# Performance work log

Hardware: AMD Instinct MI355X
Metric: run time of the kernel (lower is better)

Reference implementation:

```python
import jax, jax.numpy as jnp
import numpy as np

B, C_IN, C_OUT, L = 16, 128, 128, 1024
DK, DV, H = 32, 32, 8
SCALE = DK ** (-0.5)


def setup_inputs() -> dict:
    key = jax.random.key(0)
    ks = jax.random.split(key, 7)
    qkv_dim = H * (2 * DK + DV)
    # Conv1d with kernel_size=1 == per-position linear; store weights as (out, in)
    return {
        "x": jax.random.normal(ks[0], (B, C_IN, L), dtype=jnp.float32),
        "w_qkv": jax.random.normal(ks[1], (qkv_dim, C_IN), dtype=jnp.float32) * (C_IN ** -0.5),
        "b_qkv": jax.random.normal(ks[2], (qkv_dim,), dtype=jnp.float32) * 0.02,
        "w_o": jax.random.normal(ks[3], (C_OUT, H * DV), dtype=jnp.float32) * ((H * DV) ** -0.5),
        "b_o": jax.random.normal(ks[4], (C_OUT,), dtype=jnp.float32) * 0.02,
        "w_res": jax.random.normal(ks[5], (C_OUT, C_IN), dtype=jnp.float32) * (C_IN ** -0.5),
        "b_res": jax.random.normal(ks[6], (C_OUT,), dtype=jnp.float32) * 0.02,
    }


def reference(x, w_qkv, b_qkv, w_o, b_o, w_res, b_res):
    batch, _, seq = x.shape
    # qkv projection (1x1 conv): (B, H*(2dk+dv), L)
    qkv = jnp.einsum("oc,bcl->bol", w_qkv, x) + b_qkv[:, None]
    qkv = qkv.reshape(batch, H, 2 * DK + DV, seq)
    q = qkv[:, :, :DK]                 # (B, H, dk, L)
    k = qkv[:, :, DK:2 * DK]           # (B, H, dk, L)
    v = qkv[:, :, 2 * DK:]             # (B, H, dv, L)
    # logits = scale * q^T k : (B, H, L, L)
    logits = SCALE * jnp.einsum("bhds,bhdt->bhst", q, k)
    weights = jax.nn.softmax(logits, axis=-1)
    # z_i = (weights @ v^T)^T : (B, H, dv, L)
    z = jnp.einsum("bhst,bhdt->bhds", weights, v)
    z = z.reshape(batch, H * DV, seq)
    out = jnp.einsum("oc,bcl->bol", w_o, z) + b_o[:, None]
    out = out + jnp.einsum("oc,bcl->bol", w_res, x) + b_res[:, None]
    return out
```

## Files before the change

kernel.cpp:

```cpp
#include <hip/hip_runtime.h>

#define B_    16
#define L_    1024
#define H_    8
#define SCALE  0.17677669529663687f
#define QSCALE 0.25510940349191965f

typedef __attribute__((ext_vector_type(8))) short bf16x8;
typedef __attribute__((ext_vector_type(4))) float f32x4;
typedef unsigned short u16t;

__device__ inline u16t f2bf(float f) {
    unsigned u = __float_as_uint(f);
    u = (u + 0x7FFF + ((u >> 16) & 1)) >> 16;
    return (u16t)u;
}
__device__ inline unsigned f2bf_pk(float a, float b) {
    unsigned ua = __float_as_uint(a);
    unsigned ub = __float_as_uint(b);
    ua = (ua + 0x7FFF + ((ua >> 16) & 1)) >> 16;
    ub = (ub + 0x7FFF + ((ub >> 16) & 1)) >> 16;
    return ua | (ub << 16);
}
__device__ inline uint2 f2bf_pk4(float a, float b, float c, float d) {
    uint2 u; u.x = f2bf_pk(a, b); u.y = f2bf_pk(c, d); return u;
}
__device__ inline unsigned trunc_pk(float f0, float f1) {
    return __builtin_amdgcn_perm(__float_as_uint(f1), __float_as_uint(f0), 0x07060302u);
}

__global__ __launch_bounds__(256) void prep_kernel(
    const float* __restrict__ x, const float* __restrict__ w_qkv,
    const float* __restrict__ w_o, const float* __restrict__ w_res,
    u16t* __restrict__ xbT, u16t* __restrict__ wqb,
    u16t* __restrict__ wob, u16t* __restrict__ wrb)
{
    const int tid = threadIdx.x;
    if (blockIdx.z == 0) {
        __shared__ u16t T[64][144];
        const int b = blockIdx.y, l0 = blockIdx.x * 64;
#pragma unroll
        for (int i = 0; i < 8; i++) {
            const int c = i * 16 + (tid >> 4);
            const int l = (tid & 15) * 4;
            const float4 v = *(const float4*)(x + ((long)b * 128 + c) * 1024 + l0 + l);
            T[l + 0][c] = f2bf(v.x);
            T[l + 1][c] = f2bf(v.y);
            T[l + 2][c] = f2bf(v.z);
            T[l + 3][c] = f2bf(v.w);
        }
        __syncthreads();
#pragma unroll
        for (int i = 0; i < 4; i++) {
            const int l  = i * 16 + (tid >> 4);
            const int c0 = (tid & 15) * 8;
            *(uint4*)(xbT + ((long)b * 1024 + l0 + l) * 128 + c0) = *(const uint4*)&T[l][c0];
        }
    } else {
        const int idx = blockIdx.y * 16 + blockIdx.x;
        if (idx >= 144) return;
        const int f = idx * 1024 + tid * 4;
        const float* src; u16t* dst; int off;
        if (f < 98304)       { src = w_qkv; dst = wqb; off = f; }
        else if (f < 131072) { src = w_o;   dst = wob; off = f - 98304; }
        else                 { src = w_res; dst = wrb; off = f - 131072; }
        const float4 v = *(const float4*)(src + off);
        *(uint2*)(dst + off) = f2bf_pk4(v.x, v.y, v.z, v.w);
    }
}

__global__ __launch_bounds__(256) void qkv_gemm_kernel(
    const u16t* __restrict__ wqb, const u16t* __restrict__ xbT,
    const float* __restrict__ b_qkv,
    u16t* __restrict__ qT, u16t* __restrict__ kT, u16t* __restrict__ vN)
{
    const int lblk = blockIdx.x * 128;
    const int bh = blockIdx.y;
    const int b = bh >> 3, h = bh & 7;
    const int tid = threadIdx.x, lane = tid & 63, wv = tid >> 6;
    const int l15 = lane & 15, quad = lane >> 4;
    const int lw = lblk + wv * 32;

    f32x4 acc[6][2];
#pragma unroll
    for (int mi = 0; mi < 6; mi++)
#pragma unroll
        for (int ni = 0; ni < 2; ni++) acc[mi][ni] = (f32x4)0.f;

    const u16t* wrow = wqb + (long)h * 96 * 128;
#pragma unroll
    for (int ks = 0; ks < 4; ks++) {
        const int k0 = ks * 32 + quad * 8;
        bf16x8 af[6], bf[2];
#pragma unroll
        for (int mi = 0; mi < 6; mi++)
            af[mi] = *(const bf16x8*)(wrow + (mi * 16 + l15) * 128 + k0);
#pragma unroll
        for (int ni = 0; ni < 2; ni++)
            bf[ni] = *(const bf16x8*)(xbT + ((long)b * 1024 + lw + ni * 16 + l15) * 128 + k0);
#pragma unroll
        for (int mi = 0; mi < 6; mi++)
#pragma unroll
            for (int ni = 0; ni < 2; ni++)
                acc[mi][ni] = __builtin_amdgcn_mfma_f32_16x16x32_bf16(af[mi], bf[ni], acc[mi][ni], 0, 0, 0);
    }

    const long bh_ = bh;
#pragma unroll
    for (int mi = 0; mi < 6; mi++) {
        float bias[4];
#pragma unroll
        for (int r = 0; r < 4; r++) bias[r] = b_qkv[h * 96 + mi * 16 + quad * 4 + r];
#pragma unroll
        for (int ni = 0; ni < 2; ni++) {
            const int l = lw + ni * 16 + l15;
            const f32x4 a = acc[mi][ni];
            if (mi < 2) {
                const uint2 u = f2bf_pk4((a[0] + bias[0]) * QSCALE, (a[1] + bias[1]) * QSCALE,
                                         (a[2] + bias[2]) * QSCALE, (a[3] + bias[3]) * QSCALE);
                *(uint2*)(qT + (bh_ * 1024 + l) * 32 + mi * 16 + quad * 4) = u;
            } else if (mi < 4) {
                const uint2 u = f2bf_pk4(a[0] + bias[0], a[1] + bias[1],
                                         a[2] + bias[2], a[3] + bias[3]);
                *(uint2*)(kT + (bh_ * 1024 + l) * 32 + (mi - 2) * 16 + quad * 4) = u;
            } else {
#pragma unroll
                for (int r = 0; r < 4; r++)
                    vN[(bh_ * 32 + (mi - 4) * 16 + quad * 4 + r) * 1024 + l] = f2bf(a[r] + bias[r]);
            }
        }
    }
}

__global__ __launch_bounds__(256) void attn_kernel5(
    const u16t* __restrict__ qT, const u16t* __restrict__ kT,
    const u16t* __restrict__ vN, u16t* __restrict__ zT)
{
    __shared__ __align__(16) u16t Ps[4][2][2][16][40];

    const int bh = blockIdx.x;
    const int b = bh >> 3, h = bh & 7;
    const int sblk = blockIdx.y * 128;
    const int tid = threadIdx.x, lane = tid & 63, wv = tid >> 6;
    const int l15 = lane & 15, quad = lane >> 4;

    const int sw = sblk + wv * 32;
    bf16x8 qf[2];
    qf[0] = *(const bf16x8*)(qT + ((long)bh * 1024 + sw + l15) * 32 + quad * 8);
    qf[1] = *(const bf16x8*)(qT + ((long)bh * 1024 + sw + 16 + l15) * 32 + quad * 8);

    const u16t* kp = kT + (long)bh * 1024 * 32 + l15 * 32 + quad * 8;
    const u16t* vp = vN + (long)bh * 32 * 1024 + l15 * 1024 + quad * 8;

    f32x4 zacc[2][2];
#pragma unroll
    for (int a = 0; a < 2; a++)
#pragma unroll
        for (int c = 0; c < 2; c++) zacc[a][c] = (f32x4)0.f;
    f32x4 lacc4[2] = {(f32x4)0.f, (f32x4)0.f};

    for (int t0 = 0; t0 < L_; t0 += 64) {
        bf16x8 kf[4], vf[2][2];
#pragma unroll
        for (int tg = 0; tg < 4; tg++)
            kf[tg] = *(const bf16x8*)(kp + (t0 + tg * 16) * 32);
#pragma unroll
        for (int dt = 0; dt < 2; dt++)
#pragma unroll
            for (int tt = 0; tt < 2; tt++)
                vf[dt][tt] = *(const bf16x8*)(vp + dt * 16 * 1024 + t0 + tt * 32);

#pragma unroll
        for (int st = 0; st < 2; st++) {
#pragma unroll
            for (int tg = 0; tg < 4; tg++) {
                const f32x4 sv = __builtin_amdgcn_mfma_f32_16x16x32_bf16(kf[tg], qf[st], (f32x4)0.f, 0, 0, 0);
                f32x4 ev;
#pragma unroll
                for (int i = 0; i < 4; i++) ev[i] = __builtin_amdgcn_exp2f(sv[i]);
                lacc4[st] += ev;
                uint2 u;
                u.x = trunc_pk(ev[0], ev[1]);
                u.y = trunc_pk(ev[2], ev[3]);
                *(uint2*)&Ps[wv][st][tg >> 1][l15][(tg & 1) * 16 + quad * 4] = u;
            }
        }

#pragma unroll
        for (int st = 0; st < 2; st++) {
#pragma unroll
            for (int tt = 0; tt < 2; tt++) {
                const bf16x8 pf = *(const bf16x8*)&Ps[wv][st][tt][l15][quad * 8];
                zacc[st][0] = __builtin_amdgcn_mfma_f32_16x16x32_bf16(vf[0][tt], pf, zacc[st][0], 0, 0, 0);
                zacc[st][1] = __builtin_amdgcn_mfma_f32_16x16x32_bf16(vf[1][tt], pf, zacc[st][1], 0, 0, 0);
            }
        }
    }

#pragma unroll
    for (int st = 0; st < 2; st++) {
        float lf = (lacc4[st][0] + lacc4[st][1]) + (lacc4[st][2] + lacc4[st][3]);
        lf += __shfl_xor(lf, 16);
        lf += __shfl_xor(lf, 32);
        const float rl = 1.f / lf;
        const int s = sblk + wv * 32 + st * 16 + l15;
        u16t* zrow = zT + ((long)b * 1024 + s) * 256 + h * 32;
        const uint2 u0 = f2bf_pk4(zacc[st][0][0] * rl, zacc[st][0][1] * rl,
                                  zacc[st][0][2] * rl, zacc[st][0][3] * rl);
        *(uint2*)(zrow + quad * 4) = u0;
        const uint2 u1 = f2bf_pk4(zacc[st][1][0] * rl, zacc[st][1][1] * rl,
                                  zacc[st][1][2] * rl, zacc[st][1][3] * rl);
        *(uint2*)(zrow + 16 + quad * 4) = u1;
    }
}

__global__ __launch_bounds__(256) void out_gemm_kernel(
    const u16t* __restrict__ wob, const u16t* __restrict__ wrb,
    const u16t* __restrict__ zT, const u16t* __restrict__ xbT,
    const float* __restrict__ b_o, const float* __restrict__ b_res,
    float* __restrict__ out)
{
    const int lblk = blockIdx.x * 64, oblk = blockIdx.y * 64, b = blockIdx.z;
    const int tid = threadIdx.x, lane = tid & 63, wv = tid >> 6;
    const int wm = wv >> 1, wn = wv & 1;
    const int l15 = lane & 15, quad = lane >> 4;
    const int ow = oblk + wm * 32;
    const int lw = lblk + wn * 32;

    f32x4 acc[2][2];
#pragma unroll
    for (int a = 0; a < 2; a++)
#pragma unroll
        for (int c = 0; c < 2; c++) acc[a][c] = (f32x4)0.f;

#pragma unroll
    for (int ks = 0; ks < 8; ks++) {
        const int k0 = ks * 32 + quad * 8;
        const bf16x8 af0 = *(const bf16x8*)(wob + (ow + l15) * 256 + k0);
        const bf16x8 af1 = *(const bf16x8*)(wob + (ow + 16 + l15) * 256 + k0);
        const bf16x8 bf0 = *(const bf16x8*)(zT + ((long)b * 1024 + lw + l15) * 256 + k0);
        const bf16x8 bf1 = *(const bf16x8*)(zT + ((long)b * 1024 + lw + 16 + l15) * 256 + k0);
        acc[0][0] = __builtin_amdgcn_mfma_f32_16x16x32_bf16(af0, bf0, acc[0][0], 0, 0, 0);
        acc[0][1] = __builtin_amdgcn_mfma_f32_16x16x32_bf16(af0, bf1, acc[0][1], 0, 0, 0);
        acc[1][0] = __builtin_amdgcn_mfma_f32_16x16x32_bf16(af1, bf0, acc[1][0], 0, 0, 0);
        acc[1][1] = __builtin_amdgcn_mfma_f32_16x16x32_bf16(af1, bf1, acc[1][1], 0, 0, 0);
    }
#pragma unroll
    for (int ks = 0; ks < 4; ks++) {
        const int k0 = ks * 32 + quad * 8;
        const bf16x8 af0 = *(const bf16x8*)(wrb + (ow + l15) * 128 + k0);
        const bf16x8 af1 = *(const bf16x8*)(wrb + (ow + 16 + l15) * 128 + k0);
        const bf16x8 bf0 = *(const bf16x8*)(xbT + ((long)b * 1024 + lw + l15) * 128 + k0);
        const bf16x8 bf1 = *(const bf16x8*)(xbT + ((long)b * 1024 + lw + 16 + l15) * 128 + k0);
        acc[0][0] = __builtin_amdgcn_mfma_f32_16x16x32_bf16(af0, bf0, acc[0][0], 0, 0, 0);
        acc[0][1] = __builtin_amdgcn_mfma_f32_16x16x32_bf16(af0, bf1, acc[0][1], 0, 0, 0);
        acc[1][0] = __builtin_amdgcn_mfma_f32_16x16x32_bf16(af1, bf0, acc[1][0], 0, 0, 0);
        acc[1][1] = __builtin_amdgcn_mfma_f32_16x16x32_bf16(af1, bf1, acc[1][1], 0, 0, 0);
    }

#pragma unroll
    for (int mi = 0; mi < 2; mi++) {
#pragma unroll
        for (int r = 0; r < 4; r++) {
            const int o = ow + mi * 16 + quad * 4 + r;
            const float bias = b_o[o] + b_res[o];
#pragma unroll
            for (int ni = 0; ni < 2; ni++)
                out[((long)b * 128 + o) * 1024 + lw + ni * 16 + l15] = acc[mi][ni][r] + bias;
        }
    }
}

extern "C" void kernel_launch(void* const* d_in, const int* in_sizes, int n_in,
                              void* d_out, int out_size, void* d_ws, size_t ws_size,
                              hipStream_t stream)
{
    const float* x     = (const float*)d_in[0];
    const float* w_qkv = (const float*)d_in[1];
    const float* b_qkv = (const float*)d_in[2];
    const float* w_o   = (const float*)d_in[3];
    const float* b_o   = (const float*)d_in[4];
    const float* w_res = (const float*)d_in[5];
    const float* b_res = (const float*)d_in[6];
    float* out = (float*)d_out;

    u16t* xbT = (u16t*)d_ws;
    u16t* qT  = xbT + (size_t)2097152;
    u16t* kT  = qT  + (size_t)4194304;
    u16t* vN  = kT  + (size_t)4194304;
    u16t* zT  = vN  + (size_t)4194304;
    u16t* wqb = zT  + (size_t)4194304;
    u16t* wob = wqb + (size_t)98304;
    u16t* wrb = wob + (size_t)32768;

    prep_kernel<<<dim3(16, 16, 2), 256, 0, stream>>>(x, w_qkv, w_o, w_res, xbT, wqb, wob, wrb);
    qkv_gemm_kernel<<<dim3(8, 128, 1), 256, 0, stream>>>(wqb, xbT, b_qkv, qT, kT, vN);
    attn_kernel5<<<dim3(128, 8, 1), 256, 0, stream>>>(qT, kT, vN, zT);
    out_gemm_kernel<<<dim3(16, 2, 16), 256, 0, stream>>>(wob, wrb, zT, xbT, b_o, b_res, out);
}
```

Before: 157.0 us.

## Software-prefetch operands in qkv, attention and output GEMM loops; shrink out tile

The qkv GEMM and output GEMM now double-buffer their register operands, loading the next K-slice while MFMAs run on the current one. The attention kernel prefetches the next 64-column K/V tile into registers before doing the current tile's exp and PV work. The output GEMM tile is halved along L so twice as many blocks launch, and all three kernels get launch_bounds with a minimum of 4 blocks. The aim is to hide global-load latency and raise occupancy. In exchange, register pressure goes up, and the attention loop issues one redundant wraparound load on its last iteration.

```diff
diff --git a/kernel.cpp b/kernel.cpp
--- a/kernel.cpp
+++ b/kernel.cpp
@@ -69,7 +69,7 @@
     }
 }
 
-__global__ __launch_bounds__(256) void qkv_gemm_kernel(
+__global__ __launch_bounds__(256, 4) void qkv_gemm_kernel(
     const u16t* __restrict__ wqb, const u16t* __restrict__ xbT,
     const float* __restrict__ b_qkv,
     u16t* __restrict__ qT, u16t* __restrict__ kT, u16t* __restrict__ vN)
@@ -87,22 +87,31 @@
 #pragma unroll
         for (int ni = 0; ni < 2; ni++) acc[mi][ni] = (f32x4)0.f;
 
-    const u16t* wrow = wqb + (long)h * 96 * 128;
+    const u16t* wrow = wqb + (long)h * 96 * 128 + l15 * 128 + quad * 8;
+    const u16t* xr0  = xbT + ((long)b * 1024 + lw + l15) * 128 + quad * 8;
+    const u16t* xr1  = xr0 + 16 * 128;
+
+    bf16x8 af[2][6], bf[2][2];
+#pragma unroll
+    for (int mi = 0; mi < 6; mi++) af[0][mi] = *(const bf16x8*)(wrow + mi * 16 * 128);
+    bf[0][0] = *(const bf16x8*)(xr0);
+    bf[0][1] = *(const bf16x8*)(xr1);
+
 #pragma unroll
     for (int ks = 0; ks < 4; ks++) {
-        const int k0 = ks * 32 + quad * 8;
-        bf16x8 af[6], bf[2];
+        const int cur = ks & 1, nxt = cur ^ 1;
+        if (ks < 3) {
+            const int k0 = (ks + 1) * 32;
+#pragma unroll
+            for (int mi = 0; mi < 6; mi++) af[nxt][mi] = *(const bf16x8*)(wrow + mi * 16 * 128 + k0);
+            bf[nxt][0] = *(const bf16x8*)(xr0 + k0);
+            bf[nxt][1] = *(const bf16x8*)(xr1 + k0);
+        }
 #pragma unroll
         for (int mi = 0; mi < 6; mi++)
-            af[mi] = *(const bf16x8*)(wrow + (mi * 16 + l15) * 128 + k0);
-#pragma unroll
-        for (int ni = 0; ni < 2; ni++)
-            bf[ni] = *(const bf16x8*)(xbT + ((long)b * 1024 + lw + ni * 16 + l15) * 128 + k0);
-#pragma unroll
-        for (int mi = 0; mi < 6; mi++)
 #pragma unroll
             for (int ni = 0; ni < 2; ni++)
-                acc[mi][ni] = __builtin_amdgcn_mfma_f32_16x16x32_bf16(af[mi], bf[ni], acc[mi][ni], 0, 0, 0);
+                acc[mi][ni] = __builtin_amdgcn_mfma_f32_16x16x32_bf16(af[cur][mi], bf[cur][ni], acc[mi][ni], 0, 0, 0);
     }
 
     const long bh_ = bh;
@@ -132,7 +141,7 @@
     }
 }
 
-__global__ __launch_bounds__(256) void attn_kernel5(
+__global__ __launch_bounds__(256, 4) void attn_kernel7(
     const u16t* __restrict__ qT, const u16t* __restrict__ kT,
     const u16t* __restrict__ vN, u16t* __restrict__ zT)
 {
@@ -159,16 +168,27 @@
         for (int c = 0; c < 2; c++) zacc[a][c] = (f32x4)0.f;
     f32x4 lacc4[2] = {(f32x4)0.f, (f32x4)0.f};
 
+    bf16x8 kf[4], vf[4];
+#pragma unroll
+    for (int tg = 0; tg < 4; tg++)
+        kf[tg] = *(const bf16x8*)(kp + tg * 16 * 32);
+#pragma unroll
+    for (int dt = 0; dt < 2; dt++)
+#pragma unroll
+        for (int tt = 0; tt < 2; tt++)
+            vf[dt * 2 + tt] = *(const bf16x8*)(vp + dt * 16 * 1024 + tt * 32);
+
     for (int t0 = 0; t0 < L_; t0 += 64) {
-        bf16x8 kf[4], vf[2][2];
+        const int tn = (t0 + 64) & 1023;
+        bf16x8 nk[4], nv[4];
 #pragma unroll
         for (int tg = 0; tg < 4; tg++)
-            kf[tg] = *(const bf16x8*)(kp + (t0 + tg * 16) * 32);
+            nk[tg] = *(const bf16x8*)(kp + (tn + tg * 16) * 32);
 #pragma unroll
         for (int dt = 0; dt < 2; dt++)
 #pragma unroll
             for (int tt = 0; tt < 2; tt++)
-                vf[dt][tt] = *(const bf16x8*)(vp + dt * 16 * 1024 + t0 + tt * 32);
+                nv[dt * 2 + tt] = *(const bf16x8*)(vp + dt * 16 * 1024 + tn + tt * 32);
 
 #pragma unroll
         for (int st = 0; st < 2; st++) {
@@ -191,10 +211,13 @@
 #pragma unroll
             for (int tt = 0; tt < 2; tt++) {
                 const bf16x8 pf = *(const bf16x8*)&Ps[wv][st][tt][l15][quad * 8];
-                zacc[st][0] = __builtin_amdgcn_mfma_f32_16x16x32_bf16(vf[0][tt], pf, zacc[st][0], 0, 0, 0);
-                zacc[st][1] = __builtin_amdgcn_mfma_f32_16x16x32_bf16(vf[1][tt], pf, zacc[st][1], 0, 0, 0);
+                zacc[st][0] = __builtin_amdgcn_mfma_f32_16x16x32_bf16(vf[tt], pf, zacc[st][0], 0, 0, 0);
+                zacc[st][1] = __builtin_amdgcn_mfma_f32_16x16x32_bf16(vf[2 + tt], pf, zacc[st][1], 0, 0, 0);
             }
         }
+
+#pragma unroll
+        for (int i = 0; i < 4; i++) { kf[i] = nk[i]; vf[i] = nv[i]; }
     }
 
 #pragma unroll
@@ -214,59 +237,60 @@
     }
 }
 
-__global__ __launch_bounds__(256) void out_gemm_kernel(
+__global__ __launch_bounds__(256, 4) void out_gemm_kernel(
     const u16t* __restrict__ wob, const u16t* __restrict__ wrb,
     const u16t* __restrict__ zT, const u16t* __restrict__ xbT,
     const float* __restrict__ b_o, const float* __restrict__ b_res,
     float* __restrict__ out)
 {
-    const int lblk = blockIdx.x * 64, oblk = blockIdx.y * 64, b = blockIdx.z;
+    const int lblk = blockIdx.x * 32, oblk = blockIdx.y * 64, b = blockIdx.z;
     const int tid = threadIdx.x, lane = tid & 63, wv = tid >> 6;
     const int wm = wv >> 1, wn = wv & 1;
     const int l15 = lane & 15, quad = lane >> 4;
     const int ow = oblk + wm * 32;
-    const int lw = lblk + wn * 32;
-
-    f32x4 acc[2][2];
-#pragma unroll
-    for (int a = 0; a < 2; a++)
-#pragma unroll
-        for (int c = 0; c < 2; c++) acc[a][c] = (f32x4)0.f;
-
-#pragma unroll
-    for (int ks = 0; ks < 8; ks++) {
-        const int k0 = ks * 32 + quad * 8;
-        const bf16x8 af0 = *(const bf16x8*)(wob + (ow + l15) * 256 + k0);
-        const bf16x8 af1 = *(const bf16x8*)(wob + (ow + 16 + l15) * 256 + k0);
-        const bf16x8 bf0 = *(const bf16x8*)(zT + ((long)b * 1024 + lw + l15) * 256 + k0);
-        const bf16x8 bf1 = *(const bf16x8*)(zT + ((long)b * 1024 + lw + 16 + l15) * 256 + k0);
-        acc[0][0] = __builtin_amdgcn_mfma_f32_16x16x32_bf16(af0, bf0, acc[0][0], 0, 0, 0);
-        acc[0][1] = __builtin_amdgcn_mfma_f32_16x16x32_bf16(af0, bf1, acc[0][1], 0, 0, 0);
-        acc[1][0] = __builtin_amdgcn_mfma_f32_16x16x32_bf16(af1, bf0, acc[1][0], 0, 0, 0);
-        acc[1][1] = __builtin_amdgcn_mfma_f32_16x16x32_bf16(af1, bf1, acc[1][1], 0, 0, 0);
-    }
-#pragma unroll
-    for (int ks = 0; ks < 4; ks++) {
-        const int k0 = ks * 32 + quad * 8;
-        const bf16x8 af0 = *(const bf16x8*)(wrb + (ow + l15) * 128 + k0);
-        const bf16x8 af1 = *(const bf16x8*)(wrb + (ow + 16 + l15) * 128 + k0);
-        const bf16x8 bf0 = *(const bf16x8*)(xbT + ((long)b * 1024 + lw + l15) * 128 + k0);
-        const bf16x8 bf1 = *(const bf16x8*)(xbT + ((long)b * 1024 + lw + 16 + l15) * 128 + k0);
-        acc[0][0] = __builtin_amdgcn_mfma_f32_16x16x32_bf16(af0, bf0, acc[0][0], 0, 0, 0);
-        acc[0][1] = __builtin_amdgcn_mfma_f32_16x16x32_bf16(af0, bf1, acc[0][1], 0, 0, 0);
-        acc[1][0] = __builtin_amdgcn_mfma_f32_16x16x32_bf16(af1, bf0, acc[1][0], 0, 0, 0);
-        acc[1][1] = __builtin_amdgcn_mfma_f32_16x16x32_bf16(af1, bf1, acc[1][1], 0, 0, 0);
-    }
-
+    const int lw = lblk + wn * 16;
+
+    f32x4 acc0 = (f32x4)0.f, acc1 = (f32x4)0.f;
+
+    const u16t* zrow = zT + ((long)b * 1024 + lw + l15) * 256 + quad * 8;
+    const u16t* xrow = xbT + ((long)b * 1024 + lw + l15) * 128 + quad * 8;
+    const u16t* wo0 = wob + (ow + l15) * 256 + quad * 8;
+    const u16t* wo1 = wob + (ow + 16 + l15) * 256 + quad * 8;
+    const u16t* wr0 = wrb + (ow + l15) * 128 + quad * 8;
+    const u16t* wr1 = wrb + (ow + 16 + l15) * 128 + quad * 8;
+
+    bf16x8 af0[2], af1[2], bf[2];
+    af0[0] = *(const bf16x8*)(wo0);
+    af1[0] = *(const bf16x8*)(wo1);
+    bf[0]  = *(const bf16x8*)(zrow);
+
+#pragma unroll
+    for (int ks = 0; ks < 12; ks++) {
+        const int cur = ks & 1, nxt = cur ^ 1;
+        if (ks < 11) {
+            const int kn = ks + 1;
+            if (kn < 8) {
+                af0[nxt] = *(const bf16x8*)(wo0 + kn * 32);
+                af1[nxt] = *(const bf16x8*)(wo1 + kn * 32);
+                bf[nxt]  = *(const bf16x8*)(zrow + kn * 32);
+            } else {
+                af0[nxt] = *(const bf16x8*)(wr0 + (kn - 8) * 32);
+                af1[nxt] = *(const bf16x8*)(wr1 + (kn - 8) * 32);
+                bf[nxt]  = *(const bf16x8*)(xrow + (kn - 8) * 32);
+            }
+        }
+        acc0 = __builtin_amdgcn_mfma_f32_16x16x32_bf16(af0[cur], bf[cur], acc0, 0, 0, 0);
+        acc1 = __builtin_amdgcn_mfma_f32_16x16x32_bf16(af1[cur], bf[cur], acc1, 0, 0, 0);
+    }
+
+    const int lcol = lw + l15;
 #pragma unroll
     for (int mi = 0; mi < 2; mi++) {
+        const f32x4 a = (mi == 0) ? acc0 : acc1;
 #pragma unroll
         for (int r = 0; r < 4; r++) {
             const int o = ow + mi * 16 + quad * 4 + r;
-            const float bias = b_o[o] + b_res[o];
-#pragma unroll
-            for (int ni = 0; ni < 2; ni++)
-                out[((long)b * 128 + o) * 1024 + lw + ni * 16 + l15] = acc[mi][ni][r] + bias;
+            out[((long)b * 128 + o) * 1024 + lcol] = a[r] + b_o[o] + b_res[o];
         }
     }
 }
@@ -295,6 +319,6 @@
 
     prep_kernel<<<dim3(16, 16, 2), 256, 0, stream>>>(x, w_qkv, w_o, w_res, xbT, wqb, wob, wrb);
     qkv_gemm_kernel<<<dim3(8, 128, 1), 256, 0, stream>>>(wqb, xbT, b_qkv, qT, kT, vN);
-    attn_kernel5<<<dim3(128, 8, 1), 256, 0, stream>>>(qT, kT, vN, zT);
-    out_gemm_kernel<<<dim3(16, 2, 16), 256, 0, stream>>>(wob, wrb, zT, xbT, b_o, b_res, out);
-}
+    attn_kernel7<<<dim3(128, 8, 1), 256, 0, stream>>>(qT, kT, vN, zT);
+    out_gemm_kernel<<<dim3(32, 2, 16), 256, 0, stream>>>(wob, wrb, zT, xbT, b_o, b_res, out);
+}
```

After: 161.6 us. 1.03x slower.
